# Optimization experiments

Hardware: AMD Instinct MI355X
Metric: run time of the kernel (lower is better)

## Reference

```python
import jax, jax.numpy as jnp
import numpy as np

N_ITEMS = 512
TABLE_SAMPLES = 2048
FULL_SIZE = 32768
PADDED_SIZE = 65536
BATCH = 8
N_EVENTS = 64


def setup_inputs() -> dict:
    key = jax.random.key(0)
    k1, k2, k3 = jax.random.split(key, 3)
    selections = jax.random.normal(k1, (BATCH, N_EVENTS, N_ITEMS), dtype=jnp.float32)
    # Envelopes init: uniform(-1,1) * linspace(1,0)**uniform(50,100) per item
    base = jax.random.uniform(k2, (N_ITEMS, TABLE_SAMPLES), minval=-1.0, maxval=1.0)
    exps = jax.random.uniform(jax.random.fold_in(k2, 1), (N_ITEMS, 1), minval=50.0, maxval=100.0)
    ramp = jnp.linspace(1.0, 0.0, TABLE_SAMPLES)[None, :]
    items = (base * ramp ** exps).astype(jnp.float32)
    # postprocess multiplies by uniform(-0.02, 0.02) noise of the interpolated shape
    noise = jax.random.uniform(k3, (BATCH, N_EVENTS, FULL_SIZE), minval=-0.02, maxval=0.02, dtype=jnp.float32)
    return {"selections": selections, "items": items, "noise": noise}


def reference(selections, items, noise):
    # preprocess_items: shift/scale into [0, ~1]
    items = items - items.min()
    items = items / (items.max() + 0.001)

    # select_items(..., type='sparse_softmax'): softmax over items, keep only
    # the max entry (scaled one-hot), then weighted combine against the table.
    sm = jax.nn.softmax(selections, axis=-1)                      # [b, e, n]
    w = jnp.max(sm, axis=-1, keepdims=True)                       # [b, e, 1]
    hard = jax.nn.one_hot(jnp.argmax(sm, axis=-1), sm.shape[-1], dtype=sm.dtype)
    sel = hard * w                                                # sparse one-hot weights
    selected = jnp.einsum('ben,nt->bet', sel, items)              # [b, e, T]

    # interpolate_last_axis: linear interpolation (half-pixel centers) to FULL_SIZE
    in_size = selected.shape[-1]
    pos = (jnp.arange(FULL_SIZE, dtype=jnp.float32) + 0.5) * (in_size / FULL_SIZE) - 0.5
    pos = jnp.clip(pos, 0.0, in_size - 1)
    lo = jnp.floor(pos).astype(jnp.int32)
    hi = jnp.minimum(lo + 1, in_size - 1)
    frac = (pos - lo).astype(selected.dtype)
    amp = selected[..., lo] * (1.0 - frac) + selected[..., hi] * frac  # [b, e, FULL]

    # multiply by noise, pad to PADDED_SIZE
    amp = amp * noise
    pad = jnp.zeros(amp.shape[:-1] + (PADDED_SIZE - FULL_SIZE,), dtype=amp.dtype)
    return jnp.concatenate([amp, pad], axis=-1)                   # [b, e, PADDED]
```

## Files before the change

kernel.cpp:

```cpp
#include <hip/hip_runtime.h>
#include <math.h>

constexpr int N_ITEMS = 512;
constexpr int TS      = 2048;
constexpr int FULL    = 32768;
constexpr int PADDED  = 65536;
constexpr int NPAIR   = 512;
constexpr int SPLIT   = 4;

using f4 = __attribute__((ext_vector_type(4))) float;

__device__ __forceinline__ unsigned fenc(float f) {
    unsigned u = __float_as_uint(f);
    return (u & 0x80000000u) ? ~u : (u | 0x80000000u);
}
__device__ __forceinline__ float fdec(unsigned e) {
    return __uint_as_float((e & 0x80000000u) ? (e & 0x7FFFFFFFu) : ~e);
}


__global__ void __launch_bounds__(256) k_prep(const f4* __restrict__ items4,
                                              const float* __restrict__ sel,
                                              unsigned* __restrict__ ws_min,
                                              unsigned* __restrict__ ws_max,
                                              int* __restrict__ ws_idx,
                                              float* __restrict__ ws_w) {
    __shared__ unsigned smin[4], smax[4];
    int blk = blockIdx.x;

    if (blk < 256) {
        unsigned lmin = 0xFFFFFFFFu, lmax = 0u;
        const int NV = (N_ITEMS * TS) / 4;
        for (int i = blk * 256 + threadIdx.x; i < NV; i += 256 * 256) {
            f4 v = items4[i];
            unsigned e0 = fenc(v.x), e1 = fenc(v.y), e2 = fenc(v.z), e3 = fenc(v.w);
            lmin = min(min(min(lmin, e0), min(e1, e2)), e3);
            lmax = max(max(max(lmax, e0), max(e1, e2)), e3);
        }
        for (int off = 32; off > 0; off >>= 1) {
            lmin = min(lmin, (unsigned)__shfl_xor((int)lmin, off));
            lmax = max(lmax, (unsigned)__shfl_xor((int)lmax, off));
        }
        int wave = threadIdx.x >> 6;
        if ((threadIdx.x & 63) == 0) { smin[wave] = lmin; smax[wave] = lmax; }
        __syncthreads();
        if (threadIdx.x == 0) {
            ws_min[blk] = min(min(smin[0], smin[1]), min(smin[2], smin[3]));
            ws_max[blk] = max(max(smax[0], smax[1]), max(smax[2], smax[3]));
        }
    } else {
        int p    = (blk - 256) * 4 + (threadIdx.x >> 6);
        int lane = threadIdx.x & 63;
        const float* s = sel + (size_t)p * N_ITEMS;
        float x[8];
        float vmax = -INFINITY;
        int   imax = 0x7FFFFFFF;
        #pragma unroll
        for (int k = 0; k < 8; ++k) {
            int i = lane + k * 64;
            x[k] = s[i];
            if (x[k] > vmax) { vmax = x[k]; imax = i; }
        }
        for (int off = 32; off > 0; off >>= 1) {
            float ov = __shfl_xor(vmax, off);
            int   oi = __shfl_xor(imax, off);
            if (ov > vmax || (ov == vmax && oi < imax)) { vmax = ov; imax = oi; }
        }
        float se = 0.0f;
        #pragma unroll
        for (int k = 0; k < 8; ++k) se += expf(x[k] - vmax);
        for (int off = 32; off > 0; off >>= 1) se += __shfl_xor(se, off);
        if (lane == 0) { ws_idx[p] = imax; ws_w[p] = 1.0f / se; }
    }
}

__global__ void __launch_bounds__(256) k_main(const float* __restrict__ items,
                                              const float* __restrict__ noise,
                                              const unsigned* __restrict__ ws_min,
                                              const unsigned* __restrict__ ws_max,
                                              const int* __restrict__ ws_idx,
                                              const float* __restrict__ ws_w,
                                              float* __restrict__ out) {
    __shared__ float row[TS];
    __shared__ unsigned sred[8];
    __shared__ float s_sb[2];

    int blk = blockIdx.x;
    int p   = blk >> 2;
    int q   = blk & 3;
    int tid = threadIdx.x;

    int idx = ws_idx[p];
    const f4* it4 = (const f4*)(items + (size_t)idx * TS);
    f4 r0 = it4[tid];
    f4 r1 = it4[tid + 256];

    unsigned lmin = ws_min[tid], lmax = ws_max[tid];
    for (int off = 32; off > 0; off >>= 1) {
        lmin = min(lmin, (unsigned)__shfl_xor((int)lmin, off));
        lmax = max(lmax, (unsigned)__shfl_xor((int)lmax, off));
    }
    int wave = tid >> 6;
    if ((tid & 63) == 0) { sred[wave] = lmin; sred[4 + wave] = lmax; }
    __syncthreads();
    if (tid == 0) {
        unsigned m0 = min(min(sred[0], sred[1]), min(sred[2], sred[3]));
        unsigned m1 = max(max(sred[4], sred[5]), max(sred[6], sred[7]));
        float minv  = fdec(m0);
        float maxv  = fdec(m1);
        float denom = (maxv - minv) + 0.001f;
        float scale = ws_w[p] / denom;
        s_sb[0] = scale;
        s_sb[1] = -minv * scale;
    }
    __syncthreads();
    float scale = s_sb[0], bias = s_sb[1];

    row[tid * 4 + 0] = fmaf(r0.x, scale, bias);
    row[tid * 4 + 1] = fmaf(r0.y, scale, bias);
    row[tid * 4 + 2] = fmaf(r0.z, scale, bias);
    row[tid * 4 + 3] = fmaf(r0.w, scale, bias);
    row[(tid + 256) * 4 + 0] = fmaf(r1.x, scale, bias);
    row[(tid + 256) * 4 + 1] = fmaf(r1.y, scale, bias);
    row[(tid + 256) * 4 + 2] = fmaf(r1.z, scale, bias);
    row[(tid + 256) * 4 + 3] = fmaf(r1.w, scale, bias);
    __syncthreads();

    constexpr int CHUNK = FULL / SPLIT;
    const f4* nz4  = (const f4*)(noise + (size_t)p * FULL + (size_t)q * CHUNK);
    f4*       o4   = (f4*)(out + (size_t)p * PADDED + (size_t)q * CHUNK);
    f4*       pad4 = (f4*)(out + (size_t)p * PADDED + FULL + (size_t)q * CHUNK);
    int tbase = q * CHUNK;

    f4 z = {0.f, 0.f, 0.f, 0.f};
    for (int v = tid; v < CHUNK / 4; v += 256) {
        f4 nz = __builtin_nontemporal_load(&nz4[v]);
        f4 o;
        int t0 = tbase + v * 4;
        #pragma unroll
        for (int j = 0; j < 4; ++j) {
            float pos = ((float)(t0 + j) + 0.5f) * 0.0625f - 0.5f;
            pos = fminf(fmaxf(pos, 0.0f), (float)(TS - 1));
            int lo = (int)pos;
            int hi = min(lo + 1, TS - 1);
            float fr = pos - (float)lo;
            float amp = row[lo] * (1.0f - fr) + row[hi] * fr;
            o[j] = amp * nz[j];
        }
        __builtin_nontemporal_store(o, &o4[v]);
        __builtin_nontemporal_store(z, &pad4[v]);
    }
}

extern "C" void kernel_launch(void* const* d_in, const int* in_sizes, int n_in,
                              void* d_out, int out_size, void* d_ws, size_t ws_size,
                              hipStream_t stream) {
    const float* sel   = (const float*)d_in[0];
    const float* items = (const float*)d_in[1];
    const float* noise = (const float*)d_in[2];
    float* out = (float*)d_out;

    unsigned* ws_min = (unsigned*)d_ws;
    unsigned* ws_max = (unsigned*)((char*)d_ws + 1024);
    int*      ws_idx = (int*)((char*)d_ws + 2048);
    float*    ws_w   = (float*)((char*)d_ws + 4096);

    hipLaunchKernelGGL(k_prep, dim3(256 + NPAIR / 4), dim3(256), 0, stream,
                       (const f4*)items, sel, ws_min, ws_max, ws_idx, ws_w);
    hipLaunchKernelGGL(k_main, dim3(NPAIR * SPLIT), dim3(256), 0, stream,
                       items, noise, ws_min, ws_max, ws_idx, ws_w, out);
}
```

Baseline: 46.48 us.

## Move zero-padding stores into prep kernel and halve main kernel grid split

The zero-fill of the padded half of the output moves from the main kernel into the prep kernel. The prep grid grows to 1024 blocks, and each block writes one half of one pair's padding alongside the min/max and softmax work. The main kernel now splits each pair in 2 instead of 4, so each block loads and rescales the item row half as often and only writes interpolated data. This overlaps the pad writes with the reduction phase, but the prep kernel gets heavier and the main kernel has fewer, larger blocks.

```diff
diff --git a/kernel.cpp b/kernel.cpp
--- a/kernel.cpp
+++ b/kernel.cpp
@@ -6,7 +6,6 @@
 constexpr int FULL    = 32768;
 constexpr int PADDED  = 65536;
 constexpr int NPAIR   = 512;
-constexpr int SPLIT   = 4;
 
 using f4 = __attribute__((ext_vector_type(4))) float;
 
@@ -24,14 +23,16 @@
                                               unsigned* __restrict__ ws_min,
                                               unsigned* __restrict__ ws_max,
                                               int* __restrict__ ws_idx,
-                                              float* __restrict__ ws_w) {
+                                              float* __restrict__ ws_w,
+                                              float* __restrict__ out) {
     __shared__ unsigned smin[4], smax[4];
     int blk = blockIdx.x;
+    int tid = threadIdx.x;
 
     if (blk < 256) {
         unsigned lmin = 0xFFFFFFFFu, lmax = 0u;
         const int NV = (N_ITEMS * TS) / 4;
-        for (int i = blk * 256 + threadIdx.x; i < NV; i += 256 * 256) {
+        for (int i = blk * 256 + tid; i < NV; i += 256 * 256) {
             f4 v = items4[i];
             unsigned e0 = fenc(v.x), e1 = fenc(v.y), e2 = fenc(v.z), e3 = fenc(v.w);
             lmin = min(min(min(lmin, e0), min(e1, e2)), e3);
@@ -41,16 +42,16 @@
             lmin = min(lmin, (unsigned)__shfl_xor((int)lmin, off));
             lmax = max(lmax, (unsigned)__shfl_xor((int)lmax, off));
         }
-        int wave = threadIdx.x >> 6;
-        if ((threadIdx.x & 63) == 0) { smin[wave] = lmin; smax[wave] = lmax; }
+        int wave = tid >> 6;
+        if ((tid & 63) == 0) { smin[wave] = lmin; smax[wave] = lmax; }
         __syncthreads();
-        if (threadIdx.x == 0) {
+        if (tid == 0) {
             ws_min[blk] = min(min(smin[0], smin[1]), min(smin[2], smin[3]));
             ws_max[blk] = max(max(smax[0], smax[1]), max(smax[2], smax[3]));
         }
-    } else {
-        int p    = (blk - 256) * 4 + (threadIdx.x >> 6);
-        int lane = threadIdx.x & 63;
+    } else if (blk < 384) {
+        int p    = (blk - 256) * 4 + (tid >> 6);
+        int lane = tid & 63;
         const float* s = sel + (size_t)p * N_ITEMS;
         float x[8];
         float vmax = -INFINITY;
@@ -72,6 +73,15 @@
         for (int off = 32; off > 0; off >>= 1) se += __shfl_xor(se, off);
         if (lane == 0) { ws_idx[p] = imax; ws_w[p] = 1.0f / se; }
     }
+
+    {
+        int p = blk >> 1, h = blk & 1;
+        f4* pad4 = (f4*)(out + (size_t)p * PADDED + FULL + (size_t)h * (PADDED - FULL) / 2);
+        f4 z = {0.f, 0.f, 0.f, 0.f};
+        #pragma unroll
+        for (int v = 0; v < 16; ++v)
+            __builtin_nontemporal_store(z, &pad4[tid + v * 256]);
+    }
 }
 
 __global__ void __launch_bounds__(256) k_main(const float* __restrict__ items,
@@ -86,8 +96,8 @@
     __shared__ float s_sb[2];
 
     int blk = blockIdx.x;
-    int p   = blk >> 2;
-    int q   = blk & 3;
+    int p   = blk >> 1;
+    int q   = blk & 1;
     int tid = threadIdx.x;
 
     int idx = ws_idx[p];
@@ -126,13 +136,11 @@
     row[(tid + 256) * 4 + 3] = fmaf(r1.w, scale, bias);
     __syncthreads();
 
-    constexpr int CHUNK = FULL / SPLIT;
-    const f4* nz4  = (const f4*)(noise + (size_t)p * FULL + (size_t)q * CHUNK);
-    f4*       o4   = (f4*)(out + (size_t)p * PADDED + (size_t)q * CHUNK);
-    f4*       pad4 = (f4*)(out + (size_t)p * PADDED + FULL + (size_t)q * CHUNK);
+    constexpr int CHUNK = FULL / 2;
+    const f4* nz4 = (const f4*)(noise + (size_t)p * FULL + (size_t)q * CHUNK);
+    f4*       o4  = (f4*)(out + (size_t)p * PADDED + (size_t)q * CHUNK);
     int tbase = q * CHUNK;
 
-    f4 z = {0.f, 0.f, 0.f, 0.f};
     for (int v = tid; v < CHUNK / 4; v += 256) {
         f4 nz = __builtin_nontemporal_load(&nz4[v]);
         f4 o;
@@ -148,7 +156,6 @@
             o[j] = amp * nz[j];
         }
         __builtin_nontemporal_store(o, &o4[v]);
-        __builtin_nontemporal_store(z, &pad4[v]);
     }
 }
 
@@ -165,8 +172,8 @@
     int*      ws_idx = (int*)((char*)d_ws + 2048);
     float*    ws_w   = (float*)((char*)d_ws + 4096);
 
-    hipLaunchKernelGGL(k_prep, dim3(256 + NPAIR / 4), dim3(256), 0, stream,
-                       (const f4*)items, sel, ws_min, ws_max, ws_idx, ws_w);
-    hipLaunchKernelGGL(k_main, dim3(NPAIR * SPLIT), dim3(256), 0, stream,
+    hipLaunchKernelGGL(k_prep, dim3(NPAIR * 2), dim3(256), 0, stream,
+                       (const f4*)items, sel, ws_min, ws_max, ws_idx, ws_w, out);
+    hipLaunchKernelGGL(k_main, dim3(NPAIR * 2), dim3(256), 0, stream,
                        items, noise, ws_min, ws_max, ws_idx, ws_w, out);
 }
```

New measurement: 40.95 us. 1.14x faster.

## Drop shared-memory row staging; gather items directly and fold normalization per element

Applied to the files above, without the earlier changes.

The main kernel no longer stages the selected, normalized item row in shared memory behind two barriers. Each thread now reads the needed samples straight from global memory (three loads per output vector, cached in L1/L2) and applies the scale/bias after interpolating. The global min/max partials are cut from 256 to 64, so one wave can reduce them with shuffles and no LDS. The split per pair also drops from 4 to 2 blocks, which halves the per-block setup. The cost is redundant global gathers and fewer, longer blocks.

```diff
diff --git a/kernel.cpp b/kernel.cpp
--- a/kernel.cpp
+++ b/kernel.cpp
@@ -6,7 +6,7 @@
 constexpr int FULL    = 32768;
 constexpr int PADDED  = 65536;
 constexpr int NPAIR   = 512;
-constexpr int SPLIT   = 4;
+constexpr int NMM     = 64;
 
 using f4 = __attribute__((ext_vector_type(4))) float;
 
@@ -27,11 +27,12 @@
                                               float* __restrict__ ws_w) {
     __shared__ unsigned smin[4], smax[4];
     int blk = blockIdx.x;
+    int tid = threadIdx.x;
 
-    if (blk < 256) {
+    if (blk < NMM) {
         unsigned lmin = 0xFFFFFFFFu, lmax = 0u;
         const int NV = (N_ITEMS * TS) / 4;
-        for (int i = blk * 256 + threadIdx.x; i < NV; i += 256 * 256) {
+        for (int i = blk * 256 + tid; i < NV; i += NMM * 256) {
             f4 v = items4[i];
             unsigned e0 = fenc(v.x), e1 = fenc(v.y), e2 = fenc(v.z), e3 = fenc(v.w);
             lmin = min(min(min(lmin, e0), min(e1, e2)), e3);
@@ -41,16 +42,16 @@
             lmin = min(lmin, (unsigned)__shfl_xor((int)lmin, off));
             lmax = max(lmax, (unsigned)__shfl_xor((int)lmax, off));
         }
-        int wave = threadIdx.x >> 6;
-        if ((threadIdx.x & 63) == 0) { smin[wave] = lmin; smax[wave] = lmax; }
+        int wave = tid >> 6;
+        if ((tid & 63) == 0) { smin[wave] = lmin; smax[wave] = lmax; }
         __syncthreads();
-        if (threadIdx.x == 0) {
+        if (tid == 0) {
             ws_min[blk] = min(min(smin[0], smin[1]), min(smin[2], smin[3]));
             ws_max[blk] = max(max(smax[0], smax[1]), max(smax[2], smax[3]));
         }
     } else {
-        int p    = (blk - 256) * 4 + (threadIdx.x >> 6);
-        int lane = threadIdx.x & 63;
+        int p    = (blk - NMM) * 4 + (tid >> 6);
+        int lane = tid & 63;
         const float* s = sel + (size_t)p * N_ITEMS;
         float x[8];
         float vmax = -INFINITY;
@@ -81,52 +82,28 @@
                                               const int* __restrict__ ws_idx,
                                               const float* __restrict__ ws_w,
                                               float* __restrict__ out) {
-    __shared__ float row[TS];
-    __shared__ unsigned sred[8];
-    __shared__ float s_sb[2];
+    int blk = blockIdx.x;
+    int p   = blk >> 1;
+    int q   = blk & 1;
+    int tid = threadIdx.x;
+    int lane = tid & 63;
 
-    int blk = blockIdx.x;
-    int p   = blk >> 2;
-    int q   = blk & 3;
-    int tid = threadIdx.x;
-
-    int idx = ws_idx[p];
-    const f4* it4 = (const f4*)(items + (size_t)idx * TS);
-    f4 r0 = it4[tid];
-    f4 r1 = it4[tid + 256];
-
-    unsigned lmin = ws_min[tid], lmax = ws_max[tid];
+    unsigned lmin = ws_min[lane], lmax = ws_max[lane];
     for (int off = 32; off > 0; off >>= 1) {
         lmin = min(lmin, (unsigned)__shfl_xor((int)lmin, off));
         lmax = max(lmax, (unsigned)__shfl_xor((int)lmax, off));
     }
-    int wave = tid >> 6;
-    if ((tid & 63) == 0) { sred[wave] = lmin; sred[4 + wave] = lmax; }
-    __syncthreads();
-    if (tid == 0) {
-        unsigned m0 = min(min(sred[0], sred[1]), min(sred[2], sred[3]));
-        unsigned m1 = max(max(sred[4], sred[5]), max(sred[6], sred[7]));
-        float minv  = fdec(m0);
-        float maxv  = fdec(m1);
-        float denom = (maxv - minv) + 0.001f;
-        float scale = ws_w[p] / denom;
-        s_sb[0] = scale;
-        s_sb[1] = -minv * scale;
-    }
-    __syncthreads();
-    float scale = s_sb[0], bias = s_sb[1];
+    float minv  = fdec(lmin);
+    float maxv  = fdec(lmax);
+    float denom = (maxv - minv) + 0.001f;
+    int   idx   = ws_idx[p];
+    float w     = ws_w[p];
+    float scale = w / denom;
+    float bias  = -minv * scale;
 
-    row[tid * 4 + 0] = fmaf(r0.x, scale, bias);
-    row[tid * 4 + 1] = fmaf(r0.y, scale, bias);
-    row[tid * 4 + 2] = fmaf(r0.z, scale, bias);
-    row[tid * 4 + 3] = fmaf(r0.w, scale, bias);
-    row[(tid + 256) * 4 + 0] = fmaf(r1.x, scale, bias);
-    row[(tid + 256) * 4 + 1] = fmaf(r1.y, scale, bias);
-    row[(tid + 256) * 4 + 2] = fmaf(r1.z, scale, bias);
-    row[(tid + 256) * 4 + 3] = fmaf(r1.w, scale, bias);
-    __syncthreads();
+    const float* g = items + (size_t)idx * TS;
 
-    constexpr int CHUNK = FULL / SPLIT;
+    constexpr int CHUNK = FULL / 2;
     const f4* nz4  = (const f4*)(noise + (size_t)p * FULL + (size_t)q * CHUNK);
     f4*       o4   = (f4*)(out + (size_t)p * PADDED + (size_t)q * CHUNK);
     f4*       pad4 = (f4*)(out + (size_t)p * PADDED + FULL + (size_t)q * CHUNK);
@@ -135,17 +112,24 @@
     f4 z = {0.f, 0.f, 0.f, 0.f};
     for (int v = tid; v < CHUNK / 4; v += 256) {
         f4 nz = __builtin_nontemporal_load(&nz4[v]);
+        int t0 = tbase + v * 4;
+        float pos0  = ((float)t0 + 0.5f) * 0.0625f - 0.5f;
+        float pos0c = fminf(fmaxf(pos0, 0.0f), (float)(TS - 1));
+        int lo0 = (int)pos0c;
+        float a = g[lo0];
+        float b = g[min(lo0 + 1, TS - 1)];
+        float c = g[min(lo0 + 2, TS - 1)];
         f4 o;
-        int t0 = tbase + v * 4;
         #pragma unroll
         for (int j = 0; j < 4; ++j) {
-            float pos = ((float)(t0 + j) + 0.5f) * 0.0625f - 0.5f;
-            pos = fminf(fmaxf(pos, 0.0f), (float)(TS - 1));
-            int lo = (int)pos;
-            int hi = min(lo + 1, TS - 1);
-            float fr = pos - (float)lo;
-            float amp = row[lo] * (1.0f - fr) + row[hi] * fr;
-            o[j] = amp * nz[j];
+            float pj = fminf(fmaxf(pos0 + (float)j * 0.0625f, 0.0f), (float)(TS - 1));
+            int   lj = (int)pj;
+            float fr = pj - (float)lj;
+            bool  cr = lj > lo0;
+            float va = cr ? b : a;
+            float vb = cr ? c : b;
+            float raw = fmaf(fr, vb - va, va);
+            o[j] = fmaf(raw, scale, bias) * nz[j];
         }
         __builtin_nontemporal_store(o, &o4[v]);
         __builtin_nontemporal_store(z, &pad4[v]);
@@ -161,12 +145,12 @@
     float* out = (float*)d_out;
 
     unsigned* ws_min = (unsigned*)d_ws;
-    unsigned* ws_max = (unsigned*)((char*)d_ws + 1024);
-    int*      ws_idx = (int*)((char*)d_ws + 2048);
-    float*    ws_w   = (float*)((char*)d_ws + 4096);
+    unsigned* ws_max = (unsigned*)((char*)d_ws + 256);
+    int*      ws_idx = (int*)((char*)d_ws + 512);
+    float*    ws_w   = (float*)((char*)d_ws + 2560);
 
-    hipLaunchKernelGGL(k_prep, dim3(256 + NPAIR / 4), dim3(256), 0, stream,
+    hipLaunchKernelGGL(k_prep, dim3(NMM + NPAIR / 4), dim3(256), 0, stream,
                        (const f4*)items, sel, ws_min, ws_max, ws_idx, ws_w);
-    hipLaunchKernelGGL(k_main, dim3(NPAIR * SPLIT), dim3(256), 0, stream,
+    hipLaunchKernelGGL(k_main, dim3(NPAIR * 2), dim3(256), 0, stream,
                        items, noise, ws_min, ws_max, ws_idx, ws_w, out);
 }
```

Result: slower. 48.50 us (+4.3%).
